# Performance work log

Hardware: AMD Instinct MI355X
Metric: run time of the kernel (lower is better)

The kernel has to match this reference:

```python
import math
import jax, jax.numpy as jnp
import numpy as np

N, M, DK, DV = 4096, 4096, 512, 512

def setup_inputs() -> dict:
    key = jax.random.key(0)
    k1, k2, k3, k4, k5 = jax.random.split(key, 5)
    return {
        "query": jax.random.normal(k1, (1, N, DK), dtype=jnp.float32),
        "q_k":   jax.random.normal(k2, (1, N, DK), dtype=jnp.float32),
        "q_v":   jax.random.normal(k3, (1, N, DV), dtype=jnp.float32),
        "key":   jax.random.normal(k4, (1, M, DK), dtype=jnp.float32),
        "value": jax.random.normal(k5, (1, M, DV), dtype=jnp.float32),
    }

def reference(query, q_k, q_v, key, value):
    dk = query.shape[-1]
    # diagonal of query[0] @ q_k[0].T without materializing the NxN product
    q_att = jnp.einsum('nd,nd->n', query[0], q_k[0])[:, None]      # [N, 1]
    scores = query[0] @ key[0].T                                    # [N, M]
    scores = jnp.concatenate([scores, q_att], axis=-1)[None]        # [1, N, M+1]
    scores = scores / math.sqrt(dk + 1)
    attention = jax.nn.softmax(scores, axis=-1)                     # [1, N, M+1]
    res = attention[:, :, :-1] @ value                              # [1, N, DV]
    return q_v * q_att + res
```

## Files before the change

### kernel.cpp

```cpp
#include <hip/hip_runtime.h>

#define NQ 4096
#define MK 4096
#define DKC 512
#define DVC 512
#define SCALE 0.044151079f

typedef __attribute__((ext_vector_type(8))) short short8;
typedef __attribute__((ext_vector_type(4))) float f32x4;

__device__ __forceinline__ unsigned short f2bf(float x) {
  unsigned u = __float_as_uint(x);
  u += 0x7fffu + ((u >> 16) & 1u);
  return (unsigned short)(u >> 16);
}
__device__ __forceinline__ float bf2f(unsigned short h) {
  return __uint_as_float((unsigned)h << 16);
}

#define GLL16(g, l)                                                        \
  __builtin_amdgcn_global_load_lds(                                        \
      (const __attribute__((address_space(1))) unsigned int*)(g),          \
      (__attribute__((address_space(3))) unsigned int*)(l), 16, 0, 0)

__global__ __launch_bounds__(256) void prep_all(const float* __restrict__ query,
                                                const float* __restrict__ q_k,
                                                const float* __restrict__ key,
                                                const float* __restrict__ value,
                                                unsigned short* __restrict__ Qb,
                                                unsigned short* __restrict__ Kb,
                                                unsigned short* __restrict__ Vt,
                                                float* __restrict__ qatt) {
  int b = blockIdx.x;
  if (b < 1024) {
    int n = b * 4 + (threadIdx.x >> 6);
    int lane = threadIdx.x & 63;
    const float4* qr = (const float4*)(query + (size_t)n * DKC + lane * 8);
    const float4* kr = (const float4*)(q_k + (size_t)n * DKC + lane * 8);
    float4 a0 = qr[0], a1 = qr[1];
    float4 b0 = kr[0], b1 = kr[1];
    float dot = a0.x * b0.x + a0.y * b0.y + a0.z * b0.z + a0.w * b0.w +
                a1.x * b1.x + a1.y * b1.y + a1.z * b1.z + a1.w * b1.w;
    unsigned short h[8] = {f2bf(a0.x * SCALE), f2bf(a0.y * SCALE), f2bf(a0.z * SCALE),
                           f2bf(a0.w * SCALE), f2bf(a1.x * SCALE), f2bf(a1.y * SCALE),
                           f2bf(a1.z * SCALE), f2bf(a1.w * SCALE)};
    *(short8*)(Qb + (size_t)n * DKC + lane * 8) = *(short8*)h;
#pragma unroll
    for (int off = 1; off < 64; off <<= 1) dot += __shfl_xor(dot, off, 64);
    if (lane == 0) qatt[n] = dot;
  } else if (b < 2048) {
    int i = (b - 1024) * 256 + threadIdx.x;
    const float4* src = (const float4*)key + (size_t)i * 2;
    float4 a0 = src[0], a1 = src[1];
    unsigned short h[8] = {f2bf(a0.x), f2bf(a0.y), f2bf(a0.z), f2bf(a0.w),
                           f2bf(a1.x), f2bf(a1.y), f2bf(a1.z), f2bf(a1.w)};
    *(short8*)(Kb + (size_t)i * 8) = *(short8*)h;
  } else {
    __shared__ float t[32][33];
    int bi = b - 2048;
    int tx = threadIdx.x & 31, ty = threadIdx.x >> 5;
    int m0 = (bi & 127) * 32;
    int d0 = (bi >> 7) * 32;
#pragma unroll
    for (int i = 0; i < 4; ++i)
      t[ty + i * 8][tx] = value[(size_t)(m0 + ty + i * 8) * DVC + d0 + tx];
    __syncthreads();
#pragma unroll
    for (int i = 0; i < 4; ++i)
      Vt[(size_t)(d0 + ty + i * 8) * MK + m0 + tx] = f2bf(t[tx][ty + i * 8]);
  }
}

__global__ __launch_bounds__(256, 4) void gemm_s(const unsigned short* __restrict__ Qb,
                                                 const unsigned short* __restrict__ Kb,
                                                 unsigned short* __restrict__ S,
                                                 float* __restrict__ rowsum_part) {
  __shared__ __align__(16) char lds[33792];
  const int tid = threadIdx.x;
  const int wid = tid >> 6, lane = tid & 63, lr = lane & 15, lh = lane >> 4;
  const int wm = wid >> 1, wn = wid & 1;

  int bid = blockIdx.x;
  int swz = (bid & 7) * 128 + (bid >> 3);
  const int tm = swz >> 5, tn = swz & 31;
  const size_t m0 = (size_t)tm * 128, n0 = (size_t)tn * 128;

  f32x4 acc[4][4];
#pragma unroll
  for (int i = 0; i < 4; ++i)
#pragma unroll
    for (int j = 0; j < 4; ++j) acc[i][j] = (f32x4){0.f, 0.f, 0.f, 0.f};

  const char* abase = (const char*)Qb + m0 * 1024;
  const char* bbase = (const char*)Kb + n0 * 1024;

  for (int ks = 0; ks < 8; ++ks) {
    const int kb = ks * 128;
    {
      char* al = lds;
      char* bl = lds + 16384;
#pragma unroll
      for (int s = 0; s < 4; ++s) {
        int obase = wid * 4096 + s * 1024;
        int o = obase + lane * 16;
        int row = o >> 7;
        int colg = ((o >> 4) & 7) ^ (row & 7);
        GLL16(abase + (size_t)row * 1024 + kb + colg * 16, al + obase);
        GLL16(bbase + (size_t)row * 1024 + kb + colg * 16, bl + obase);
      }
    }
    __syncthreads();
#pragma unroll
    for (int kk = 0; kk < 2; ++kk) {
      short8 af[4], bf[4];
#pragma unroll
      for (int i = 0; i < 4; ++i) {
        int ar = wm * 64 + i * 16 + lr;
        af[i] = *(const short8*)(lds + ar * 128 + ((((kk << 2) + lh) ^ (lr & 7)) << 4));
        int br = wn * 64 + i * 16 + lr;
        bf[i] = *(const short8*)(lds + 16384 + br * 128 + ((((kk << 2) + lh) ^ (lr & 7)) << 4));
      }
#pragma unroll
      for (int i = 0; i < 4; ++i)
#pragma unroll
        for (int j = 0; j < 4; ++j)
          acc[i][j] = __builtin_amdgcn_mfma_f32_16x16x32_bf16(af[i], bf[j], acc[i][j], 0, 0, 0);
    }
    __syncthreads();
  }

  unsigned short* sl = (unsigned short*)lds;
  float* rs = (float*)(lds + 32768);
  float rsum[4][4];
#pragma unroll
  for (int i = 0; i < 4; ++i)
#pragma unroll
    for (int r = 0; r < 4; ++r) rsum[i][r] = 0.f;
#pragma unroll
  for (int i = 0; i < 4; ++i)
#pragma unroll
    for (int j = 0; j < 4; ++j)
#pragma unroll
      for (int r = 0; r < 4; ++r) {
        int m = wm * 64 + i * 16 + lh * 4 + r;
        int n = wn * 64 + j * 16 + lr;
        float e = __expf(acc[i][j][r]);
        sl[m * 128 + n] = f2bf(e);
        rsum[i][r] += e;
      }
#pragma unroll
  for (int i = 0; i < 4; ++i)
#pragma unroll
    for (int r = 0; r < 4; ++r) {
      float v = rsum[i][r];
      v += __shfl_xor(v, 1, 64);
      v += __shfl_xor(v, 2, 64);
      v += __shfl_xor(v, 4, 64);
      v += __shfl_xor(v, 8, 64);
      if (lr == 0) rs[wn * 128 + wm * 64 + i * 16 + lh * 4 + r] = v;
    }
  __syncthreads();
  if (tid < 128) rowsum_part[(size_t)tn * NQ + m0 + tid] = rs[tid] + rs[128 + tid];
#pragma unroll
  for (int i = 0; i < 8; ++i) {
    int o = i * 4096 + tid * 16;
    int row = o >> 8, colb = o & 255;
    *(uint4*)((char*)S + (m0 + row) * 8192 + n0 * 2 + colb) = *(const uint4*)((const char*)sl + o);
  }
}

__global__ __launch_bounds__(256, 2) void gemm_o_part(const unsigned short* __restrict__ P,
                                                      const unsigned short* __restrict__ Vt,
                                                      unsigned short* __restrict__ part) {
  __shared__ __align__(16) char lds[65536];
  const int tid = threadIdx.x;
  const int wid = tid >> 6, lane = tid & 63, lr = lane & 15, lh = lane >> 4;
  const int wm = wid >> 1, wn = wid & 1;

  int bid = blockIdx.x;
  int swz = (bid & 7) * 64 + (bid >> 3);
  const int mt = swz >> 4;
  const int nt = (swz >> 2) & 3;
  const int ksl = swz & 3;
  const size_t m0 = (size_t)mt * 128, n0 = (size_t)nt * 128;

  f32x4 acc[4][4];
#pragma unroll
  for (int i = 0; i < 4; ++i)
#pragma unroll
    for (int j = 0; j < 4; ++j) acc[i][j] = (f32x4){0.f, 0.f, 0.f, 0.f};

  const char* abase = (const char*)P + m0 * 8192 + (size_t)ksl * 2048;
  const char* bbase = (const char*)Vt + n0 * 8192 + (size_t)ksl * 2048;

  for (int ks = 0; ks < 8; ++ks) {
    const int kb = ks * 256;
    {
      char* al = lds;
      char* bl = lds + 32768;
#pragma unroll
      for (int s = 0; s < 8; ++s) {
        int obase = wid * 8192 + s * 1024;
        int o = obase + lane * 16;
        int row = o >> 8;
        int colg = ((o >> 4) & 15) ^ (row & 7);
        GLL16(abase + (size_t)row * 8192 + kb + colg * 16, al + obase);
        GLL16(bbase + (size_t)row * 8192 + kb + colg * 16, bl + obase);
      }
    }
    __syncthreads();
#pragma unroll
    for (int kk = 0; kk < 4; ++kk) {
      short8 af[4], bf[4];
#pragma unroll
      for (int i = 0; i < 4; ++i) {
        int ar = wm * 64 + i * 16 + lr;
        af[i] = *(const short8*)(lds + ar * 256 + ((((kk << 2) + lh) ^ (ar & 7)) << 4));
        int br = wn * 64 + i * 16 + lr;
        bf[i] = *(const short8*)(lds + 32768 + br * 256 + ((((kk << 2) + lh) ^ (br & 7)) << 4));
      }
#pragma unroll
      for (int i = 0; i < 4; ++i)
#pragma unroll
        for (int j = 0; j < 4; ++j)
          acc[i][j] = __builtin_amdgcn_mfma_f32_16x16x32_bf16(af[i], bf[j], acc[i][j], 0, 0, 0);
    }
    __syncthreads();
  }

  unsigned short* sl = (unsigned short*)lds;
#pragma unroll
  for (int i = 0; i < 4; ++i)
#pragma unroll
    for (int j = 0; j < 4; ++j)
#pragma unroll
      for (int r = 0; r < 4; ++r) {
        int m = wm * 64 + i * 16 + lh * 4 + r;
        int n = wn * 64 + j * 16 + lr;
        sl[m * 128 + n] = f2bf(acc[i][j][r]);
      }
  __syncthreads();
  char* pbase = (char*)part + (size_t)ksl * NQ * DVC * 2;
#pragma unroll
  for (int i = 0; i < 8; ++i) {
    int o = i * 4096 + tid * 16;
    int row = o >> 8, colb = o & 255;
    *(uint4*)(pbase + (m0 + row) * 1024 + n0 * 2 + colb) = *(const uint4*)((const char*)sl + o);
  }
}

__global__ __launch_bounds__(256) void combine2(const unsigned short* __restrict__ part,
                                                const float* __restrict__ rowsum_part,
                                                const float* __restrict__ qatt,
                                                const float* __restrict__ q_v,
                                                float* __restrict__ out) {
  __shared__ float inv_s[4];
  const int b = blockIdx.x;
  const int t = threadIdx.x;
  if (t < 128) {
    int r = t >> 5, p = t & 31;
    float v = rowsum_part[(size_t)p * NQ + b * 4 + r];
#pragma unroll
    for (int off = 1; off < 32; off <<= 1) v += __shfl_xor(v, off, 32);
    if (p == 0) inv_s[r] = 1.0f / (v + __expf(qatt[b * 4 + r] * SCALE));
  }
  __syncthreads();
  int r = t >> 6;
  int d8 = (t & 63) * 8;
  int n = b * 4 + r;
  float qa = qatt[n];
  float iv = inv_s[r];
  size_t off = (size_t)n * DVC + d8;
  float rr[8] = {0.f, 0.f, 0.f, 0.f, 0.f, 0.f, 0.f, 0.f};
#pragma unroll
  for (int w = 0; w < 4; ++w) {
    short8 po = *(const short8*)(part + (size_t)w * NQ * DVC + off);
#pragma unroll
    for (int j = 0; j < 8; ++j) rr[j] += bf2f((unsigned short)po[j]);
  }
  const float4* qv = (const float4*)(q_v + off);
  float4 qv0 = qv[0], qv1 = qv[1];
  float4 o0 = {qv0.x * qa + rr[0] * iv, qv0.y * qa + rr[1] * iv, qv0.z * qa + rr[2] * iv,
               qv0.w * qa + rr[3] * iv};
  float4 o1 = {qv1.x * qa + rr[4] * iv, qv1.y * qa + rr[5] * iv, qv1.z * qa + rr[6] * iv,
               qv1.w * qa + rr[7] * iv};
  float4* op = (float4*)(out + off);
  op[0] = o0;
  op[1] = o1;
}

extern "C" void kernel_launch(void* const* d_in, const int* in_sizes, int n_in,
                              void* d_out, int out_size, void* d_ws, size_t ws_size,
                              hipStream_t stream) {
  const float* query = (const float*)d_in[0];
  const float* q_k = (const float*)d_in[1];
  const float* q_v = (const float*)d_in[2];
  const float* key = (const float*)d_in[3];
  const float* value = (const float*)d_in[4];
  float* out = (float*)d_out;

  char* ws = (char*)d_ws;
  unsigned short* Qb = (unsigned short*)(ws);
  unsigned short* Kb = (unsigned short*)(ws + (4u << 20));
  unsigned short* Vt = (unsigned short*)(ws + (8u << 20));
  unsigned short* S = (unsigned short*)(ws + (12u << 20));
  float* qatt = (float*)(ws + (44u << 20));
  unsigned short* part = (unsigned short*)(ws + (45u << 20));
  float* rowsum_part = (float*)(ws + (61u << 20));

  prep_all<<<dim3(4096), dim3(256), 0, stream>>>(query, q_k, key, value, Qb, Kb, Vt, qatt);
  gemm_s<<<dim3(1024), dim3(256), 0, stream>>>(Qb, Kb, S, rowsum_part);
  gemm_o_part<<<dim3(512), dim3(256), 0, stream>>>(S, Vt, part);
  combine2<<<dim3(1024), dim3(256), 0, stream>>>(part, rowsum_part, qatt, q_v, out);
}
```

Baseline: 66.97 us.

## Rewrite score GEMM as 256x256 tile with 8 waves and double-buffered LDS pipeline

Enlarges the QK^T score GEMM tile from 128x128 with 4 waves to 256x256 with 8 waves, using 128KB of LDS double-buffered across K-steps. Global-to-LDS loads for the next K-slice are interleaved between MFMA phases, with explicit barriers, setprio, and vmcnt waits to overlap memory with compute. The aim is less global traffic per FLOP and hidden load latency. The trade-offs are fewer blocks (256 on a GPU with many CUs), so occupancy drops to one block per CU, and more register pressure. The combine kernel is updated for 16 row-sum partials instead of 32.

```diff
diff --git a/kernel.cpp b/kernel.cpp
--- a/kernel.cpp
+++ b/kernel.cpp
@@ -71,100 +71,238 @@
   }
 }
 
-__global__ __launch_bounds__(256, 4) void gemm_s(const unsigned short* __restrict__ Qb,
+#define PHASE_PRE()                                         \
+  asm volatile("" ::: "memory");                            \
+  __builtin_amdgcn_s_barrier();                             \
+  asm volatile("s_waitcnt lgkmcnt(0)" ::: "memory");        \
+  __builtin_amdgcn_sched_barrier(0);                        \
+  __builtin_amdgcn_s_setprio(1)
+#define PHASE_POST()                                        \
+  __builtin_amdgcn_s_setprio(0);                            \
+  asm volatile("" ::: "memory");                            \
+  __builtin_amdgcn_s_barrier();                             \
+  asm volatile("" ::: "memory")
+
+__global__ __launch_bounds__(512, 2) void gemm_s(const unsigned short* __restrict__ Qb,
                                                  const unsigned short* __restrict__ Kb,
                                                  unsigned short* __restrict__ S,
                                                  float* __restrict__ rowsum_part) {
-  __shared__ __align__(16) char lds[33792];
+  __shared__ __align__(16) char lds[135168];
   const int tid = threadIdx.x;
   const int wid = tid >> 6, lane = tid & 63, lr = lane & 15, lh = lane >> 4;
-  const int wm = wid >> 1, wn = wid & 1;
+  const int wm = wid >> 2, wn = wid & 3;
 
   int bid = blockIdx.x;
-  int swz = (bid & 7) * 128 + (bid >> 3);
-  const int tm = swz >> 5, tn = swz & 31;
-  const size_t m0 = (size_t)tm * 128, n0 = (size_t)tn * 128;
-
-  f32x4 acc[4][4];
-#pragma unroll
-  for (int i = 0; i < 4; ++i)
-#pragma unroll
-    for (int j = 0; j < 4; ++j) acc[i][j] = (f32x4){0.f, 0.f, 0.f, 0.f};
+  int swz = (bid & 7) * 32 + (bid >> 3);
+  const int tm = swz >> 4, tn = swz & 15;
+  const size_t m0 = (size_t)tm * 256, n0 = (size_t)tn * 256;
 
   const char* abase = (const char*)Qb + m0 * 1024;
   const char* bbase = (const char*)Kb + n0 * 1024;
 
-  for (int ks = 0; ks < 8; ++ks) {
-    const int kb = ks * 128;
-    {
-      char* al = lds;
-      char* bl = lds + 16384;
-#pragma unroll
-      for (int s = 0; s < 4; ++s) {
-        int obase = wid * 4096 + s * 1024;
-        int o = obase + lane * 16;
-        int row = o >> 7;
-        int colg = ((o >> 4) & 7) ^ (row & 7);
-        GLL16(abase + (size_t)row * 1024 + kb + colg * 16, al + obase);
-        GLL16(bbase + (size_t)row * 1024 + kb + colg * 16, bl + obase);
+  auto stg = [&](const char* xbase, int kt, int h, int db, int boff) {
+    char* dst = lds + db * 65536 + boff + h * 16384;
+    const char* src = xbase + (size_t)(h * 128) * 1024 + kt * 128;
+#pragma unroll
+    for (int s = 0; s < 2; ++s) {
+      int obase = wid * 2048 + s * 1024;
+      int o = obase + lane * 16;
+      int row = o >> 7;
+      int g = ((o >> 4) & 7) ^ (row & 7);
+      GLL16(src + (size_t)row * 1024 + g * 16, dst + obase);
+    }
+  };
+  auto ard = [&](int fi, int ks, int db) -> short8 {
+    return *(const short8*)(lds + db * 65536 + wm * 16384 + (fi * 16 + lr) * 128 +
+                            ((((ks << 2) + lh) ^ (lr & 7)) << 4));
+  };
+  auto brd = [&](int fj, int ks, int db) -> short8 {
+    return *(const short8*)(lds + db * 65536 + 32768 + (wn >> 1) * 16384 +
+                            ((wn & 1) * 64 + fj * 16 + lr) * 128 +
+                            ((((ks << 2) + lh) ^ (lr & 7)) << 4));
+  };
+
+  f32x4 acc[8][4];
+#pragma unroll
+  for (int i = 0; i < 8; ++i)
+#pragma unroll
+    for (int j = 0; j < 4; ++j) acc[i][j] = (f32x4){0.f, 0.f, 0.f, 0.f};
+  short8 a[8][2], b[4][2];
+
+  stg(abase, 0, 0, 0, 0);
+  stg(abase, 0, 1, 0, 0);
+  stg(bbase, 0, 0, 0, 32768);
+  stg(bbase, 0, 1, 0, 32768);
+  stg(abase, 1, 0, 1, 0);
+  asm volatile("s_waitcnt vmcnt(2)" ::: "memory");
+  __builtin_amdgcn_s_barrier();
+  asm volatile("" ::: "memory");
+
+  for (int it = 0; it < 4; ++it) {
+    const int kt1 = 2 * it + 1;
+    const bool more = (it < 3);
+#pragma unroll
+    for (int fi = 0; fi < 4; ++fi)
+#pragma unroll
+      for (int ks = 0; ks < 2; ++ks) a[fi][ks] = ard(fi, ks, 0);
+#pragma unroll
+    for (int fj = 0; fj < 2; ++fj)
+#pragma unroll
+      for (int ks = 0; ks < 2; ++ks) b[fj][ks] = brd(fj, ks, 0);
+    stg(abase, kt1, 1, 1, 0);
+    PHASE_PRE();
+#pragma unroll
+    for (int fi = 0; fi < 4; ++fi)
+#pragma unroll
+      for (int fj = 0; fj < 2; ++fj)
+#pragma unroll
+        for (int ks = 0; ks < 2; ++ks)
+          acc[fi][fj] = __builtin_amdgcn_mfma_f32_16x16x32_bf16(a[fi][ks], b[fj][ks], acc[fi][fj], 0, 0, 0);
+    PHASE_POST();
+#pragma unroll
+    for (int fj = 2; fj < 4; ++fj)
+#pragma unroll
+      for (int ks = 0; ks < 2; ++ks) b[fj][ks] = brd(fj, ks, 0);
+    stg(bbase, kt1, 0, 1, 32768);
+    PHASE_PRE();
+#pragma unroll
+    for (int fi = 0; fi < 4; ++fi)
+#pragma unroll
+      for (int fj = 2; fj < 4; ++fj)
+#pragma unroll
+        for (int ks = 0; ks < 2; ++ks)
+          acc[fi][fj] = __builtin_amdgcn_mfma_f32_16x16x32_bf16(a[fi][ks], b[fj][ks], acc[fi][fj], 0, 0, 0);
+    PHASE_POST();
+#pragma unroll
+    for (int fi = 4; fi < 8; ++fi)
+#pragma unroll
+      for (int ks = 0; ks < 2; ++ks) a[fi][ks] = ard(fi, ks, 0);
+    stg(bbase, kt1, 1, 1, 32768);
+    PHASE_PRE();
+#pragma unroll
+    for (int fi = 4; fi < 8; ++fi)
+#pragma unroll
+      for (int fj = 2; fj < 4; ++fj)
+#pragma unroll
+        for (int ks = 0; ks < 2; ++ks)
+          acc[fi][fj] = __builtin_amdgcn_mfma_f32_16x16x32_bf16(a[fi][ks], b[fj][ks], acc[fi][fj], 0, 0, 0);
+    PHASE_POST();
+    if (more) stg(abase, 2 * it + 2, 0, 0, 0);
+    PHASE_PRE();
+#pragma unroll
+    for (int fi = 4; fi < 8; ++fi)
+#pragma unroll
+      for (int fj = 0; fj < 2; ++fj)
+#pragma unroll
+        for (int ks = 0; ks < 2; ++ks)
+          acc[fi][fj] = __builtin_amdgcn_mfma_f32_16x16x32_bf16(a[fi][ks], b[fj][ks], acc[fi][fj], 0, 0, 0);
+    __builtin_amdgcn_s_setprio(0);
+    if (more) asm volatile("s_waitcnt vmcnt(2)" ::: "memory");
+    else      asm volatile("s_waitcnt vmcnt(0)" ::: "memory");
+    asm volatile("" ::: "memory");
+    __builtin_amdgcn_s_barrier();
+    asm volatile("" ::: "memory");
+#pragma unroll
+    for (int fi = 0; fi < 4; ++fi)
+#pragma unroll
+      for (int ks = 0; ks < 2; ++ks) a[fi][ks] = ard(fi, ks, 1);
+#pragma unroll
+    for (int fj = 0; fj < 2; ++fj)
+#pragma unroll
+      for (int ks = 0; ks < 2; ++ks) b[fj][ks] = brd(fj, ks, 1);
+    if (more) stg(abase, 2 * it + 2, 1, 0, 0);
+    PHASE_PRE();
+#pragma unroll
+    for (int fi = 0; fi < 4; ++fi)
+#pragma unroll
+      for (int fj = 0; fj < 2; ++fj)
+#pragma unroll
+        for (int ks = 0; ks < 2; ++ks)
+          acc[fi][fj] = __builtin_amdgcn_mfma_f32_16x16x32_bf16(a[fi][ks], b[fj][ks], acc[fi][fj], 0, 0, 0);
+    PHASE_POST();
+#pragma unroll
+    for (int fj = 2; fj < 4; ++fj)
+#pragma unroll
+      for (int ks = 0; ks < 2; ++ks) b[fj][ks] = brd(fj, ks, 1);
+    if (more) stg(bbase, 2 * it + 2, 0, 0, 32768);
+    PHASE_PRE();
+#pragma unroll
+    for (int fi = 0; fi < 4; ++fi)
+#pragma unroll
+      for (int fj = 2; fj < 4; ++fj)
+#pragma unroll
+        for (int ks = 0; ks < 2; ++ks)
+          acc[fi][fj] = __builtin_amdgcn_mfma_f32_16x16x32_bf16(a[fi][ks], b[fj][ks], acc[fi][fj], 0, 0, 0);
+    PHASE_POST();
+#pragma unroll
+    for (int fi = 4; fi < 8; ++fi)
+#pragma unroll
+      for (int ks = 0; ks < 2; ++ks) a[fi][ks] = ard(fi, ks, 1);
+    if (more) stg(bbase, 2 * it + 2, 1, 0, 32768);
+    PHASE_PRE();
+#pragma unroll
+    for (int fi = 4; fi < 8; ++fi)
+#pragma unroll
+      for (int fj = 2; fj < 4; ++fj)
+#pragma unroll
+        for (int ks = 0; ks < 2; ++ks)
+          acc[fi][fj] = __builtin_amdgcn_mfma_f32_16x16x32_bf16(a[fi][ks], b[fj][ks], acc[fi][fj], 0, 0, 0);
+    PHASE_POST();
+    if (more) stg(abase, 2 * it + 3, 0, 1, 0);
+    PHASE_PRE();
+#pragma unroll
+    for (int fi = 4; fi < 8; ++fi)
+#pragma unroll
+      for (int fj = 0; fj < 2; ++fj)
+#pragma unroll
+        for (int ks = 0; ks < 2; ++ks)
+          acc[fi][fj] = __builtin_amdgcn_mfma_f32_16x16x32_bf16(a[fi][ks], b[fj][ks], acc[fi][fj], 0, 0, 0);
+    __builtin_amdgcn_s_setprio(0);
+    if (more) asm volatile("s_waitcnt vmcnt(2)" ::: "memory");
+    asm volatile("" ::: "memory");
+    __builtin_amdgcn_s_barrier();
+    asm volatile("" ::: "memory");
+  }
+
+  unsigned short* sl = (unsigned short*)lds;
+  float* rs = (float*)(lds + 131072);
+  float rsum[8][4];
+#pragma unroll
+  for (int fi = 0; fi < 8; ++fi)
+#pragma unroll
+    for (int r = 0; r < 4; ++r) rsum[fi][r] = 0.f;
+#pragma unroll
+  for (int fi = 0; fi < 8; ++fi)
+#pragma unroll
+    for (int fj = 0; fj < 4; ++fj)
+#pragma unroll
+      for (int r = 0; r < 4; ++r) {
+        int m = wm * 128 + fi * 16 + lh * 4 + r;
+        int n = wn * 64 + fj * 16 + lr;
+        float e = __expf(acc[fi][fj][r]);
+        sl[m * 256 + n] = f2bf(e);
+        rsum[fi][r] += e;
       }
-    }
-    __syncthreads();
-#pragma unroll
-    for (int kk = 0; kk < 2; ++kk) {
-      short8 af[4], bf[4];
-#pragma unroll
-      for (int i = 0; i < 4; ++i) {
-        int ar = wm * 64 + i * 16 + lr;
-        af[i] = *(const short8*)(lds + ar * 128 + ((((kk << 2) + lh) ^ (lr & 7)) << 4));
-        int br = wn * 64 + i * 16 + lr;
-        bf[i] = *(const short8*)(lds + 16384 + br * 128 + ((((kk << 2) + lh) ^ (lr & 7)) << 4));
-      }
-#pragma unroll
-      for (int i = 0; i < 4; ++i)
-#pragma unroll
-        for (int j = 0; j < 4; ++j)
-          acc[i][j] = __builtin_amdgcn_mfma_f32_16x16x32_bf16(af[i], bf[j], acc[i][j], 0, 0, 0);
-    }
-    __syncthreads();
-  }
-
-  unsigned short* sl = (unsigned short*)lds;
-  float* rs = (float*)(lds + 32768);
-  float rsum[4][4];
-#pragma unroll
-  for (int i = 0; i < 4; ++i)
-#pragma unroll
-    for (int r = 0; r < 4; ++r) rsum[i][r] = 0.f;
-#pragma unroll
-  for (int i = 0; i < 4; ++i)
-#pragma unroll
-    for (int j = 0; j < 4; ++j)
-#pragma unroll
-      for (int r = 0; r < 4; ++r) {
-        int m = wm * 64 + i * 16 + lh * 4 + r;
-        int n = wn * 64 + j * 16 + lr;
-        float e = __expf(acc[i][j][r]);
-        sl[m * 128 + n] = f2bf(e);
-        rsum[i][r] += e;
-      }
-#pragma unroll
-  for (int i = 0; i < 4; ++i)
+#pragma unroll
+  for (int fi = 0; fi < 8; ++fi)
 #pragma unroll
     for (int r = 0; r < 4; ++r) {
-      float v = rsum[i][r];
+      float v = rsum[fi][r];
       v += __shfl_xor(v, 1, 64);
       v += __shfl_xor(v, 2, 64);
       v += __shfl_xor(v, 4, 64);
       v += __shfl_xor(v, 8, 64);
-      if (lr == 0) rs[wn * 128 + wm * 64 + i * 16 + lh * 4 + r] = v;
+      if (lr == 0) rs[wn * 256 + wm * 128 + fi * 16 + lh * 4 + r] = v;
     }
   __syncthreads();
-  if (tid < 128) rowsum_part[(size_t)tn * NQ + m0 + tid] = rs[tid] + rs[128 + tid];
-#pragma unroll
-  for (int i = 0; i < 8; ++i) {
-    int o = i * 4096 + tid * 16;
-    int row = o >> 8, colb = o & 255;
+  if (tid < 256) {
+    float s = rs[tid] + rs[256 + tid] + rs[512 + tid] + rs[768 + tid];
+    rowsum_part[(size_t)tn * NQ + m0 + tid] = s;
+  }
+#pragma unroll
+  for (int i = 0; i < 16; ++i) {
+    int o = i * 8192 + tid * 16;
+    int row = o >> 9, colb = o & 511;
     *(uint4*)((char*)S + (m0 + row) * 8192 + n0 * 2 + colb) = *(const uint4*)((const char*)sl + o);
   }
 }
@@ -257,11 +395,13 @@
   __shared__ float inv_s[4];
   const int b = blockIdx.x;
   const int t = threadIdx.x;
-  if (t < 128) {
-    int r = t >> 5, p = t & 31;
+  if (t < 64) {
+    int r = t >> 4, p = t & 15;
     float v = rowsum_part[(size_t)p * NQ + b * 4 + r];
-#pragma unroll
-    for (int off = 1; off < 32; off <<= 1) v += __shfl_xor(v, off, 32);
+    v += __shfl_xor(v, 1, 64);
+    v += __shfl_xor(v, 2, 64);
+    v += __shfl_xor(v, 4, 64);
+    v += __shfl_xor(v, 8, 64);
     if (p == 0) inv_s[r] = 1.0f / (v + __expf(qatt[b * 4 + r] * SCALE));
   }
   __syncthreads();
@@ -309,7 +449,7 @@
   float* rowsum_part = (float*)(ws + (61u << 20));
 
   prep_all<<<dim3(4096), dim3(256), 0, stream>>>(query, q_k, key, value, Qb, Kb, Vt, qatt);
-  gemm_s<<<dim3(1024), dim3(256), 0, stream>>>(Qb, Kb, S, rowsum_part);
+  gemm_s<<<dim3(256), dim3(512), 0, stream>>>(Qb, Kb, S, rowsum_part);
   gemm_o_part<<<dim3(512), dim3(256), 0, stream>>>(S, Vt, part);
   combine2<<<dim3(1024), dim3(256), 0, stream>>>(part, rowsum_part, qatt, q_v, out);
 }
```

Result: no change. 67.74 us (+1.2%).
